# Kernel optimization log

Measured on AMD Instinct MI355X. Metric: run time of the kernel, lower is better.

## Reference

```python
import jax, jax.numpy as jnp
import numpy as np

N = 50000
R = 8
E = 100000
D_IN = 768
D_H = 256
LN_EPS = 1e-5


def _layer_norm(h, g, b):
    mu = jnp.mean(h, axis=-1, keepdims=True)
    var = jnp.mean((h - mu) ** 2, axis=-1, keepdims=True)
    return (h - mu) * jax.lax.rsqrt(var + LN_EPS) * g + b


def _rgcn_layer(x, node_w, edge_src, edge_tgt, W_rel, W_self_w, W_self_b, ln_g, ln_b):
    # x: [N, d_in]; edge_src/edge_tgt: [R, E]; W_rel: [R, d_in, d_out]
    n = x.shape[0]
    out = x @ W_self_w + W_self_b  # self loop
    for r in range(W_rel.shape[0]):  # fixed, small relation count
        src = edge_src[r]
        tgt = edge_tgt[r]
        feats = x[src] * node_w[src][:, None]          # gather + nuclearity scale, [E, d_in]
        msg = feats @ W_rel[r]                          # per-relation linear, [E, d_out]
        agg = jax.ops.segment_sum(msg, tgt, num_segments=n)                 # scatter_add
        cnt = jax.ops.segment_sum(jnp.ones(src.shape[0], x.dtype), tgt, num_segments=n)
        out = out + agg / jnp.clip(cnt, 1.0)[:, None]  # mean over relation neighbors
    return _layer_norm(jax.nn.relu(out), ln_g, ln_b)   # dropout = identity (eval)


def setup_inputs() -> dict:
    key = jax.random.key(0)
    ks = jax.random.split(key, 10)
    x = jax.random.normal(ks[0], (N, D_IN), dtype=jnp.float32)
    node_weights = jax.random.uniform(ks[1], (N,), dtype=jnp.float32)
    edge_src = jax.random.randint(ks[2], (R, E), 0, N, dtype=jnp.int32)
    edge_tgt = jax.random.randint(ks[3], (R, E), 0, N, dtype=jnp.int32)
    W_rel0 = jax.random.normal(ks[4], (R, D_IN, D_H), dtype=jnp.float32) / np.sqrt(D_IN)
    W_self0_w = jax.random.normal(ks[5], (D_IN, D_H), dtype=jnp.float32) / np.sqrt(D_IN)
    W_self0_b = jnp.zeros((D_H,), jnp.float32)
    W_rel1 = jax.random.normal(ks[6], (R, D_H, D_H), dtype=jnp.float32) / np.sqrt(D_H)
    W_self1_w = jax.random.normal(ks[7], (D_H, D_H), dtype=jnp.float32) / np.sqrt(D_H)
    W_self1_b = jnp.zeros((D_H,), jnp.float32)
    ones = jnp.ones((D_H,), jnp.float32)
    zeros = jnp.zeros((D_H,), jnp.float32)
    return {
        "x": x, "node_weights": node_weights,
        "edge_src": edge_src, "edge_tgt": edge_tgt,
        "W_rel0": W_rel0, "W_self0_w": W_self0_w, "W_self0_b": W_self0_b,
        "ln0_g": ones, "ln0_b": zeros,
        "W_rel1": W_rel1, "W_self1_w": W_self1_w, "W_self1_b": W_self1_b,
        "ln1_g": ones, "ln1_b": zeros,
    }


def reference(x, node_weights, edge_src, edge_tgt,
              W_rel0, W_self0_w, W_self0_b, ln0_g, ln0_b,
              W_rel1, W_self1_w, W_self1_b, ln1_g, ln1_b):
    h = _rgcn_layer(x, node_weights, edge_src, edge_tgt,
                    W_rel0, W_self0_w, W_self0_b, ln0_g, ln0_b)
    h = _rgcn_layer(h, node_weights, edge_src, edge_tgt,
                    W_rel1, W_self1_w, W_self1_b, ln1_g, ln1_b)
    return h  # [N, 256]
```

## Files before the change

kernel.cpp:

```cpp
#include <hip/hip_runtime.h>
#include <stdint.h>

#define N_NODES 50000
#define M_PAD   50048
#define R_REL   8
#define E_EDGES 100000
#define D_IN    768
#define D_H     256
#define N_CAT   2304
#define LN_EPS  1e-5f

#define TILES_N 18
#define TILES_M 391
#define T_TOT   (TILES_N * TILES_M)
#define T_PER_XCD ((T_TOT + 7) / 8)
#define NCHUNK  49

typedef __attribute__((ext_vector_type(8))) __bf16        bf16x8;
typedef __attribute__((ext_vector_type(4))) float         f32x4;
typedef __attribute__((ext_vector_type(8))) unsigned short u16x8;
typedef __attribute__((ext_vector_type(4))) unsigned short u16x4;
typedef __attribute__((ext_vector_type(4))) int            i32x4;

__device__ __forceinline__ float bf2f(unsigned short u) {
  union { float f; uint32_t i; } c; c.i = ((uint32_t)u) << 16; return c.f;
}
__device__ __forceinline__ unsigned short f2bf(float f) {
  uint32_t x = __float_as_uint(f);
  uint32_t r = (x + 0x7fffu + ((x >> 16) & 1u)) >> 16;
  return (unsigned short)r;
}

__device__ __forceinline__ void gload_lds16(const void* g, uint32_t lds_off) {
  __builtin_amdgcn_global_load_lds(
      (const __attribute__((address_space(1))) void*)(uintptr_t)g,
      (__attribute__((address_space(3))) void*)(uintptr_t)lds_off, 16, 0, 0);
}

__global__ void k_deg(const int* __restrict__ tgt, int* __restrict__ deg) {
  int e = blockIdx.x * 256 + threadIdx.x;
  if (e >= R_REL * E_EDGES) return;
  int r = e / E_EDGES;
  atomicAdd(&deg[r * N_NODES + tgt[e]], 1);
}

__global__ __launch_bounds__(256)
void k_scan1(const int* __restrict__ deg, int* __restrict__ rowptr,
             int* __restrict__ bsum) {
  __shared__ int wtot[4];
  const int r = blockIdx.y, chunk = blockIdx.x, tid = threadIdx.x;
  const int wave = tid >> 6, lane = tid & 63;
  const int i0 = chunk * 1024 + tid * 4;
  int v0 = 0, v1 = 0, v2 = 0, v3 = 0;
  const int* d = deg + r * N_NODES;
  if (chunk != NCHUNK - 1) {
    i32x4 v = *(const i32x4*)(d + i0);
    v0 = v[0]; v1 = v[1]; v2 = v[2]; v3 = v[3];
  } else {
    if (i0 + 0 < N_NODES) v0 = d[i0 + 0];
    if (i0 + 1 < N_NODES) v1 = d[i0 + 1];
    if (i0 + 2 < N_NODES) v2 = d[i0 + 2];
    if (i0 + 3 < N_NODES) v3 = d[i0 + 3];
  }
  const int tsum = v0 + v1 + v2 + v3;
  int inc = tsum;
#pragma unroll
  for (int off = 1; off < 64; off <<= 1) {
    int t = __shfl_up(inc, off, 64);
    if (lane >= off) inc += t;
  }
  if (lane == 63) wtot[wave] = inc;
  __syncthreads();
  int woff = 0;
#pragma unroll
  for (int w = 0; w < 4; ++w) woff += (w < wave) ? wtot[w] : 0;
  int excl = woff + inc - tsum;
  int* rp = rowptr + r * (N_NODES + 1);
  if (i0 + 0 < N_NODES) rp[i0 + 0] = excl;
  if (i0 + 1 < N_NODES) rp[i0 + 1] = excl + v0;
  if (i0 + 2 < N_NODES) rp[i0 + 2] = excl + v0 + v1;
  if (i0 + 3 < N_NODES) rp[i0 + 3] = excl + v0 + v1 + v2;
  if (tid == 0) bsum[r * NCHUNK + chunk] = wtot[0] + wtot[1] + wtot[2] + wtot[3];
}

__global__ __launch_bounds__(512)
void k_scan2(const int* __restrict__ bsum, int* __restrict__ chunkoff,
             int* __restrict__ rowptr) {
  const int r = threadIdx.x >> 6, lane = threadIdx.x & 63;
  int v = (lane < NCHUNK) ? bsum[r * NCHUNK + lane] : 0;
  int inc = v;
#pragma unroll
  for (int off = 1; off < 64; off <<= 1) {
    int t = __shfl_up(inc, off, 64);
    if (lane >= off) inc += t;
  }
  if (lane < NCHUNK) chunkoff[r * NCHUNK + lane] = inc - v;
  if (lane == NCHUNK - 1) rowptr[r * (N_NODES + 1) + N_NODES] = inc;
}

__global__ __launch_bounds__(256)
void k_scan3(const int* __restrict__ chunkoff, int* __restrict__ rowptr) {
  const int r = blockIdx.y, chunk = blockIdx.x;
  if (chunk == 0) return;
  const int off = chunkoff[r * NCHUNK + chunk];
  const int i0 = chunk * 1024 + threadIdx.x * 4;
  int* rp = rowptr + r * (N_NODES + 1);
#pragma unroll
  for (int j = 0; j < 4; ++j)
    if (i0 + j < N_NODES) rp[i0 + j] += off;
}

__global__ void k_fill(const int* __restrict__ src, const int* __restrict__ tgt,
                       const float* __restrict__ nw, const int* __restrict__ rowptr,
                       int* __restrict__ cursor, int2* __restrict__ e2) {
  int e = blockIdx.x * 256 + threadIdx.x;
  if (e >= R_REL * E_EDGES) return;
  int r = e / E_EDGES;
  int t = tgt[e], s = src[e];
  int pos = atomicAdd(&cursor[r * N_NODES + t], 1);
  int slot = r * E_EDGES + rowptr[r * (N_NODES + 1) + t] + pos;
  e2[slot] = make_int2(s, __float_as_int(nw[s]));
}

__global__ void k_cvt_x(const float* __restrict__ x, unsigned short* __restrict__ xb) {
  const size_t i = ((size_t)blockIdx.x * 256 + threadIdx.x) * 4;
  if (i >= (size_t)N_NODES * D_IN) return;
  const f32x4 v = *(const f32x4*)(x + i);
  u16x4 o = { f2bf(v[0]), f2bf(v[1]), f2bf(v[2]), f2bf(v[3]) };
  *(u16x4*)(xb + i) = o;
}

__global__ void k_cvt_w(const float* __restrict__ Ws, const float* __restrict__ Wr,
                        unsigned short* __restrict__ Wt, int K) {
  int idx = blockIdx.x * 256 + threadIdx.x;
  if (idx >= N_CAT * K) return;
  int n = idx / K, k = idx - n * K;
  float v = (n < 256) ? Ws[k * 256 + n]
                      : Wr[(size_t)((n - 256) >> 8) * K * 256 + k * 256 + (n & 255)];
  Wt[idx] = f2bf(v);
}

__global__ __launch_bounds__(256, 2)
void k_gemm(const unsigned short* __restrict__ A, const unsigned short* __restrict__ Bt,
            unsigned short* __restrict__ C, int K) {
  const int tile = (blockIdx.x & 7) * T_PER_XCD + (blockIdx.x >> 3);
  if (tile >= T_TOT) return;
  const int tileM = (tile / TILES_N) * 128;
  const int tileN = (tile % TILES_N) * 128;

  __shared__ __align__(16) char smem[32768];
  const int tid  = threadIdx.x;
  const int wave = tid >> 6, lane = tid & 63;
  const int wm = (wave >> 1) * 64, wn = (wave & 1) * 64;

  f32x4 acc[4][4] = {};

  const int srow = wave * 32 + (lane >> 2);
  const int kchunk = ((lane & 3) - ((lane >> 2) & 3)) & 3;
  const unsigned short* gA = A  + (size_t)(tileM + srow) * K + kchunk * 8;
  const unsigned short* gB = Bt + (size_t)(tileN + srow) * K + kchunk * 8;
  const uint32_t ldsA = (uint32_t)(uintptr_t)smem;
  const uint32_t ldsB = ldsA + 8192;
  const uint32_t lA0 = ldsA + (wave * 32) * 64;
  const uint32_t lB0 = ldsB + (wave * 32) * 64;
  const size_t rowstep = (size_t)16 * K;

  const int slot = (((lane >> 4) + (lane & 3)) & 3) * 16;
  const char* pA = smem        + (wm + (lane & 15)) * 64 + slot;
  const char* pB = smem + 8192 + (wn + (lane & 15)) * 64 + slot;

  const int nk = K >> 5;
  for (int kt = 0; kt < nk; ++kt) {
    const int koff = kt * 32;
    __syncthreads();
    gload_lds16(gA + koff,           lA0);
    gload_lds16(gA + rowstep + koff, lA0 + 16 * 64);
    gload_lds16(gB + koff,           lB0);
    gload_lds16(gB + rowstep + koff, lB0 + 16 * 64);
    __syncthreads();
    bf16x8 af[4], bfr[4];
#pragma unroll
    for (int i = 0; i < 4; ++i) af[i]  = *(const bf16x8*)(pA + i * 1024);
#pragma unroll
    for (int j = 0; j < 4; ++j) bfr[j] = *(const bf16x8*)(pB + j * 1024);
#pragma unroll
    for (int i = 0; i < 4; ++i)
#pragma unroll
      for (int j = 0; j < 4; ++j)
        acc[i][j] = __builtin_amdgcn_mfma_f32_16x16x32_bf16(af[i], bfr[j], acc[i][j], 0, 0, 0);
  }

  __syncthreads();
  unsigned short* st = (unsigned short*)smem + wave * 4096;
  const int rq = (lane >> 4) * 4, cq = lane & 15;
#pragma unroll
  for (int i = 0; i < 4; ++i)
#pragma unroll
    for (int j = 0; j < 4; ++j)
#pragma unroll
      for (int p = 0; p < 4; ++p)
        st[(i * 16 + rq + p) * 64 + j * 16 + cq] = f2bf(acc[i][j][p]);
  __syncthreads();
#pragma unroll
  for (int pass = 0; pass < 8; ++pass) {
    const int row = pass * 8 + (lane >> 3);
    u16x8 v = *(const u16x8*)(st + row * 64 + (lane & 7) * 8);
    size_t off = (size_t)(tileM + wm + row) * N_CAT + tileN + wn + (lane & 7) * 8;
    *(u16x8*)(C + off) = v;
  }
}

template <int FINAL>
__global__ __launch_bounds__(256)
void k_gather_ln(const unsigned short* __restrict__ Y, const int* __restrict__ rowptr,
                 const int2* __restrict__ e2, const float* __restrict__ bias,
                 const float* __restrict__ g, const float* __restrict__ bln,
                 void* __restrict__ out) {
  const int wave = threadIdx.x >> 6, lane = threadIdx.x & 63;
  const int t = blockIdx.x * 4 + wave;
  if (t >= N_NODES) return;
  const int c0 = lane * 4;

  float a0, a1, a2, a3;
  {
    u16x4 sv = *(const u16x4*)(Y + (size_t)t * N_CAT + c0);
    a0 = bf2f(sv[0]) + bias[c0 + 0];
    a1 = bf2f(sv[1]) + bias[c0 + 1];
    a2 = bf2f(sv[2]) + bias[c0 + 2];
    a3 = bf2f(sv[3]) + bias[c0 + 3];
  }
#pragma unroll
  for (int r = 0; r < R_REL; ++r) {
    const int rp0 = rowptr[r * (N_NODES + 1) + t];
    const int rp1 = rowptr[r * (N_NODES + 1) + t + 1];
    if (rp0 == rp1) continue;
    float r0 = 0, r1 = 0, r2 = 0, r3 = 0;
    float q0 = 0, q1 = 0, q2 = 0, q3 = 0;
    const int base = r * E_EDGES;
    const size_t colr = (size_t)(1 + r) * 256 + c0;
    int idx = rp0;
    for (; idx + 2 <= rp1; idx += 2) {
      const int2 p0 = e2[base + idx];
      const int2 p1 = e2[base + idx + 1];
      const float w0 = __int_as_float(p0.y);
      const float w1 = __int_as_float(p1.y);
      u16x4 v0 = *(const u16x4*)(Y + (size_t)p0.x * N_CAT + colr);
      u16x4 v1 = *(const u16x4*)(Y + (size_t)p1.x * N_CAT + colr);
      r0 += w0 * bf2f(v0[0]); r1 += w0 * bf2f(v0[1]);
      r2 += w0 * bf2f(v0[2]); r3 += w0 * bf2f(v0[3]);
      q0 += w1 * bf2f(v1[0]); q1 += w1 * bf2f(v1[1]);
      q2 += w1 * bf2f(v1[2]); q3 += w1 * bf2f(v1[3]);
    }
    if (idx < rp1) {
      const int2 p0 = e2[base + idx];
      const float w0 = __int_as_float(p0.y);
      u16x4 v0 = *(const u16x4*)(Y + (size_t)p0.x * N_CAT + colr);
      r0 += w0 * bf2f(v0[0]); r1 += w0 * bf2f(v0[1]);
      r2 += w0 * bf2f(v0[2]); r3 += w0 * bf2f(v0[3]);
    }
    const float inv = 1.0f / (float)(rp1 - rp0);
    a0 += inv * (r0 + q0); a1 += inv * (r1 + q1);
    a2 += inv * (r2 + q2); a3 += inv * (r3 + q3);
  }
  a0 = fmaxf(a0, 0.f); a1 = fmaxf(a1, 0.f); a2 = fmaxf(a2, 0.f); a3 = fmaxf(a3, 0.f);

  float s1 = a0 + a1 + a2 + a3;
#pragma unroll
  for (int off = 32; off > 0; off >>= 1) s1 += __shfl_xor(s1, off, 64);
  const float mu = s1 * (1.f / 256.f);
  const float d0 = a0 - mu, d1 = a1 - mu, d2 = a2 - mu, d3 = a3 - mu;
  float s2 = d0 * d0 + d1 * d1 + d2 * d2 + d3 * d3;
#pragma unroll
  for (int off = 32; off > 0; off >>= 1) s2 += __shfl_xor(s2, off, 64);
  const float rs = rsqrtf(s2 * (1.f / 256.f) + LN_EPS);
  const float o0 = d0 * rs * g[c0 + 0] + bln[c0 + 0];
  const float o1 = d1 * rs * g[c0 + 1] + bln[c0 + 1];
  const float o2 = d2 * rs * g[c0 + 2] + bln[c0 + 2];
  const float o3 = d3 * rs * g[c0 + 3] + bln[c0 + 3];
  if (FINAL) {
    f32x4 o = { o0, o1, o2, o3 };
    *(f32x4*)((float*)out + (size_t)t * 256 + c0) = o;
  } else {
    u16x4 o = { f2bf(o0), f2bf(o1), f2bf(o2), f2bf(o3) };
    *(u16x4*)((unsigned short*)out + (size_t)t * 256 + c0) = o;
  }
}

extern "C" void kernel_launch(void* const* d_in, const int* in_sizes, int n_in,
                              void* d_out, int out_size, void* d_ws, size_t ws_size,
                              hipStream_t stream) {
  (void)in_sizes; (void)n_in; (void)out_size; (void)ws_size;
  const float* x   = (const float*)d_in[0];
  const float* nw  = (const float*)d_in[1];
  const int*   esrc = (const int*)d_in[2];
  const int*   etgt = (const int*)d_in[3];
  const float* Wr0 = (const float*)d_in[4];
  const float* Ws0 = (const float*)d_in[5];
  const float* Wb0 = (const float*)d_in[6];
  const float* g0  = (const float*)d_in[7];
  const float* b0  = (const float*)d_in[8];
  const float* Wr1 = (const float*)d_in[9];
  const float* Ws1 = (const float*)d_in[10];
  const float* Wb1 = (const float*)d_in[11];
  const float* g1  = (const float*)d_in[12];
  const float* b1  = (const float*)d_in[13];

  char* p = (char*)d_ws;
  auto carve = [&](size_t bytes) {
    char* q = p;
    p += (bytes + 511) & ~(size_t)511;
    return q;
  };
  unsigned short* Y   = (unsigned short*)carve((size_t)M_PAD * N_CAT * 2);
  unsigned short* xb  = (unsigned short*)carve((size_t)M_PAD * D_IN * 2);
  unsigned short* h   = (unsigned short*)carve((size_t)M_PAD * D_H * 2);
  unsigned short* Wt0 = (unsigned short*)carve((size_t)N_CAT * D_IN * 2);
  unsigned short* Wt1 = (unsigned short*)carve((size_t)N_CAT * D_H * 2);
  int*   deg     = (int*)carve((size_t)R_REL * N_NODES * 4);
  int*   cursor  = (int*)carve((size_t)R_REL * N_NODES * 4);
  int*   rowptr  = (int*)carve((size_t)R_REL * (N_NODES + 1) * 4);
  int*   bsum    = (int*)carve((size_t)R_REL * NCHUNK * 4);
  int*   chunkoff= (int*)carve((size_t)R_REL * NCHUNK * 4);
  int2*  e2      = (int2*)carve((size_t)R_REL * E_EDGES * 8);

  hipMemsetAsync(deg, 0, (size_t)R_REL * N_NODES * 4, stream);
  hipMemsetAsync(cursor, 0, (size_t)R_REL * N_NODES * 4, stream);
  k_deg<<<(R_REL * E_EDGES + 255) / 256, 256, 0, stream>>>(etgt, deg);
  k_scan1<<<dim3(NCHUNK, R_REL), 256, 0, stream>>>(deg, rowptr, bsum);
  k_scan2<<<1, 512, 0, stream>>>(bsum, chunkoff, rowptr);
  k_scan3<<<dim3(NCHUNK, R_REL), 256, 0, stream>>>(chunkoff, rowptr);
  k_fill<<<(R_REL * E_EDGES + 255) / 256, 256, 0, stream>>>(esrc, etgt, nw, rowptr,
                                                            cursor, e2);
  k_cvt_x<<<(N_NODES * D_IN / 4 + 255) / 256, 256, 0, stream>>>(x, xb);
  k_cvt_w<<<(N_CAT * D_IN + 255) / 256, 256, 0, stream>>>(Ws0, Wr0, Wt0, D_IN);
  k_cvt_w<<<(N_CAT * D_H + 255) / 256, 256, 0, stream>>>(Ws1, Wr1, Wt1, D_H);

  const int nblk = 8 * T_PER_XCD;
  k_gemm<<<nblk, 256, 0, stream>>>(xb, Wt0, Y, D_IN);
  k_gather_ln<0><<<N_NODES / 4, 256, 0, stream>>>(Y, rowptr, e2, Wb0, g0, b0, h);
  k_gemm<<<nblk, 256, 0, stream>>>(h, Wt1, Y, D_H);
  k_gather_ln<1><<<N_NODES / 4, 256, 0, stream>>>(Y, rowptr, e2, Wb1, g1, b1, d_out);
}
```

Measured before the change: 894.7 us.

## Split gather wave into edge halves, pack row offsets, pad GEMM epilogue LDS

The gather/LayerNorm kernel now splits each wave into two halves. Each half processes alternate edges with 16-byte loads covering 8 columns per lane, and the halves are combined with one cross-half shuffle. A new prep kernel packs per-node (rowptr, degree) pairs for all relations contiguously, so each node reads its offsets from one cache line instead of strided rowptr arrays. The GEMM epilogue pads the LDS staging stride to 68 to avoid bank conflicts and drops a block-wide barrier, since each wave only reads back its own region. This adds one small kernel and a little LDS, and the half-wave split leaves half the lanes idle on edge-poor relations.

Measured after the change: 918.7 us. 1.03x slower.

```diff
diff --git a/kernel.cpp b/kernel.cpp
--- a/kernel.cpp
+++ b/kernel.cpp
@@ -15,6 +15,7 @@
 #define T_TOT   (TILES_N * TILES_M)
 #define T_PER_XCD ((T_TOT + 7) / 8)
 #define NCHUNK  49
+#define EP_STRIDE 68
 
 typedef __attribute__((ext_vector_type(8))) __bf16        bf16x8;
 typedef __attribute__((ext_vector_type(4))) float         f32x4;
@@ -110,6 +111,14 @@
     if (i0 + j < N_NODES) rp[i0 + j] += off;
 }
 
+__global__ void k_prep(const int* __restrict__ rowptr, const int* __restrict__ deg,
+                       int2* __restrict__ sc) {
+  int i = blockIdx.x * 256 + threadIdx.x;
+  if (i >= N_NODES * 8) return;
+  int t = i >> 3, r = i & 7;
+  sc[i] = make_int2(rowptr[r * (N_NODES + 1) + t], deg[r * N_NODES + t]);
+}
+
 __global__ void k_fill(const int* __restrict__ src, const int* __restrict__ tgt,
                        const float* __restrict__ nw, const int* __restrict__ rowptr,
                        int* __restrict__ cursor, int2* __restrict__ e2) {
@@ -148,7 +157,7 @@
   const int tileM = (tile / TILES_N) * 128;
   const int tileN = (tile % TILES_N) * 128;
 
-  __shared__ __align__(16) char smem[32768];
+  __shared__ __align__(16) char smem[34816];
   const int tid  = threadIdx.x;
   const int wave = tid >> 6, lane = tid & 63;
   const int wm = (wave >> 1) * 64, wn = (wave & 1) * 64;
@@ -191,7 +200,7 @@
   }
 
   __syncthreads();
-  unsigned short* st = (unsigned short*)smem + wave * 4096;
+  unsigned short* st = (unsigned short*)smem + wave * (64 * EP_STRIDE);
   const int rq = (lane >> 4) * 4, cq = lane & 15;
 #pragma unroll
   for (int i = 0; i < 4; ++i)
@@ -199,12 +208,14 @@
     for (int j = 0; j < 4; ++j)
 #pragma unroll
       for (int p = 0; p < 4; ++p)
-        st[(i * 16 + rq + p) * 64 + j * 16 + cq] = f2bf(acc[i][j][p]);
-  __syncthreads();
+        st[(i * 16 + rq + p) * EP_STRIDE + j * 16 + cq] = f2bf(acc[i][j][p]);
 #pragma unroll
   for (int pass = 0; pass < 8; ++pass) {
     const int row = pass * 8 + (lane >> 3);
-    u16x8 v = *(const u16x8*)(st + row * 64 + (lane & 7) * 8);
+    const unsigned short* rp_ = st + row * EP_STRIDE + (lane & 7) * 8;
+    u16x4 lo = *(const u16x4*)(rp_);
+    u16x4 hi = *(const u16x4*)(rp_ + 4);
+    u16x8 v = { lo[0], lo[1], lo[2], lo[3], hi[0], hi[1], hi[2], hi[3] };
     size_t off = (size_t)(tileM + wm + row) * N_CAT + tileN + wn + (lane & 7) * 8;
     *(u16x8*)(C + off) = v;
   }
@@ -212,77 +223,85 @@
 
 template <int FINAL>
 __global__ __launch_bounds__(256)
-void k_gather_ln(const unsigned short* __restrict__ Y, const int* __restrict__ rowptr,
+void k_gather_ln(const unsigned short* __restrict__ Y, const int2* __restrict__ sc,
                  const int2* __restrict__ e2, const float* __restrict__ bias,
                  const float* __restrict__ g, const float* __restrict__ bln,
                  void* __restrict__ out) {
   const int wave = threadIdx.x >> 6, lane = threadIdx.x & 63;
   const int t = blockIdx.x * 4 + wave;
   if (t >= N_NODES) return;
-  const int c0 = lane * 4;
-
-  float a0, a1, a2, a3;
-  {
-    u16x4 sv = *(const u16x4*)(Y + (size_t)t * N_CAT + c0);
-    a0 = bf2f(sv[0]) + bias[c0 + 0];
-    a1 = bf2f(sv[1]) + bias[c0 + 1];
-    a2 = bf2f(sv[2]) + bias[c0 + 2];
-    a3 = bf2f(sv[3]) + bias[c0 + 3];
-  }
+  const int h = lane >> 5, sl = lane & 31;
+  const int c0 = sl * 8;
+
+  float a[8];
+  if (h == 0) {
+    u16x8 sv = *(const u16x8*)(Y + (size_t)t * N_CAT + c0);
+#pragma unroll
+    for (int i = 0; i < 8; ++i) a[i] = bf2f(sv[i]);
+  } else {
+    f32x4 b0 = *(const f32x4*)(bias + c0);
+    f32x4 b1 = *(const f32x4*)(bias + c0 + 4);
+    a[0] = b0[0]; a[1] = b0[1]; a[2] = b0[2]; a[3] = b0[3];
+    a[4] = b1[0]; a[5] = b1[1]; a[6] = b1[2]; a[7] = b1[3];
+  }
+
 #pragma unroll
   for (int r = 0; r < R_REL; ++r) {
-    const int rp0 = rowptr[r * (N_NODES + 1) + t];
-    const int rp1 = rowptr[r * (N_NODES + 1) + t + 1];
-    if (rp0 == rp1) continue;
-    float r0 = 0, r1 = 0, r2 = 0, r3 = 0;
-    float q0 = 0, q1 = 0, q2 = 0, q3 = 0;
-    const int base = r * E_EDGES;
+    const int2 s = sc[t * 8 + r];
+    if (s.y == 0) continue;
+    const int base = r * E_EDGES + s.x;
     const size_t colr = (size_t)(1 + r) * 256 + c0;
-    int idx = rp0;
-    for (; idx + 2 <= rp1; idx += 2) {
-      const int2 p0 = e2[base + idx];
-      const int2 p1 = e2[base + idx + 1];
-      const float w0 = __int_as_float(p0.y);
-      const float w1 = __int_as_float(p1.y);
-      u16x4 v0 = *(const u16x4*)(Y + (size_t)p0.x * N_CAT + colr);
-      u16x4 v1 = *(const u16x4*)(Y + (size_t)p1.x * N_CAT + colr);
-      r0 += w0 * bf2f(v0[0]); r1 += w0 * bf2f(v0[1]);
-      r2 += w0 * bf2f(v0[2]); r3 += w0 * bf2f(v0[3]);
-      q0 += w1 * bf2f(v1[0]); q1 += w1 * bf2f(v1[1]);
-      q2 += w1 * bf2f(v1[2]); q3 += w1 * bf2f(v1[3]);
+    float acc[8] = {0, 0, 0, 0, 0, 0, 0, 0};
+    for (int idx = h; idx < s.y; idx += 2) {
+      const int2 p = e2[base + idx];
+      const float w = __int_as_float(p.y);
+      u16x8 v = *(const u16x8*)(Y + (size_t)p.x * N_CAT + colr);
+#pragma unroll
+      for (int i = 0; i < 8; ++i) acc[i] += w * bf2f(v[i]);
     }
-    if (idx < rp1) {
-      const int2 p0 = e2[base + idx];
-      const float w0 = __int_as_float(p0.y);
-      u16x4 v0 = *(const u16x4*)(Y + (size_t)p0.x * N_CAT + colr);
-      r0 += w0 * bf2f(v0[0]); r1 += w0 * bf2f(v0[1]);
-      r2 += w0 * bf2f(v0[2]); r3 += w0 * bf2f(v0[3]);
+    const float inv = 1.0f / (float)s.y;
+#pragma unroll
+    for (int i = 0; i < 8; ++i) a[i] += inv * acc[i];
+  }
+
+#pragma unroll
+  for (int i = 0; i < 8; ++i) {
+    a[i] += __shfl_xor(a[i], 32, 64);
+    a[i] = fmaxf(a[i], 0.f);
+  }
+  float s1 = ((a[0] + a[1]) + (a[2] + a[3])) + ((a[4] + a[5]) + (a[6] + a[7]));
+#pragma unroll
+  for (int off = 16; off > 0; off >>= 1) s1 += __shfl_xor(s1, off, 64);
+  const float mu = s1 * (1.f / 256.f);
+  float d[8], s2 = 0.f;
+#pragma unroll
+  for (int i = 0; i < 8; ++i) { d[i] = a[i] - mu; s2 += d[i] * d[i]; }
+#pragma unroll
+  for (int off = 16; off > 0; off >>= 1) s2 += __shfl_xor(s2, off, 64);
+  const float rs = rsqrtf(s2 * (1.f / 256.f) + LN_EPS);
+
+  f32x4 g0 = *(const f32x4*)(g + c0);
+  f32x4 g1 = *(const f32x4*)(g + c0 + 4);
+  f32x4 l0 = *(const f32x4*)(bln + c0);
+  f32x4 l1 = *(const f32x4*)(bln + c0 + 4);
+  float o[8];
+  o[0] = d[0] * rs * g0[0] + l0[0]; o[1] = d[1] * rs * g0[1] + l0[1];
+  o[2] = d[2] * rs * g0[2] + l0[2]; o[3] = d[3] * rs * g0[3] + l0[3];
+  o[4] = d[4] * rs * g1[0] + l1[0]; o[5] = d[5] * rs * g1[1] + l1[1];
+  o[6] = d[6] * rs * g1[2] + l1[2]; o[7] = d[7] * rs * g1[3] + l1[3];
+
+  if (h == 0) {
+    if (FINAL) {
+      float* op = (float*)out + (size_t)t * 256 + c0;
+      f32x4 v0 = { o[0], o[1], o[2], o[3] };
+      f32x4 v1 = { o[4], o[5], o[6], o[7] };
+      *(f32x4*)(op) = v0;
+      *(f32x4*)(op + 4) = v1;
+    } else {
+      u16x8 v = { f2bf(o[0]), f2bf(o[1]), f2bf(o[2]), f2bf(o[3]),
+                  f2bf(o[4]), f2bf(o[5]), f2bf(o[6]), f2bf(o[7]) };
+      *(u16x8*)((unsigned short*)out + (size_t)t * 256 + c0) = v;
     }
-    const float inv = 1.0f / (float)(rp1 - rp0);
-    a0 += inv * (r0 + q0); a1 += inv * (r1 + q1);
-    a2 += inv * (r2 + q2); a3 += inv * (r3 + q3);
-  }
-  a0 = fmaxf(a0, 0.f); a1 = fmaxf(a1, 0.f); a2 = fmaxf(a2, 0.f); a3 = fmaxf(a3, 0.f);
-
-  float s1 = a0 + a1 + a2 + a3;
-#pragma unroll
-  for (int off = 32; off > 0; off >>= 1) s1 += __shfl_xor(s1, off, 64);
-  const float mu = s1 * (1.f / 256.f);
-  const float d0 = a0 - mu, d1 = a1 - mu, d2 = a2 - mu, d3 = a3 - mu;
-  float s2 = d0 * d0 + d1 * d1 + d2 * d2 + d3 * d3;
-#pragma unroll
-  for (int off = 32; off > 0; off >>= 1) s2 += __shfl_xor(s2, off, 64);
-  const float rs = rsqrtf(s2 * (1.f / 256.f) + LN_EPS);
-  const float o0 = d0 * rs * g[c0 + 0] + bln[c0 + 0];
-  const float o1 = d1 * rs * g[c0 + 1] + bln[c0 + 1];
-  const float o2 = d2 * rs * g[c0 + 2] + bln[c0 + 2];
-  const float o3 = d3 * rs * g[c0 + 3] + bln[c0 + 3];
-  if (FINAL) {
-    f32x4 o = { o0, o1, o2, o3 };
-    *(f32x4*)((float*)out + (size_t)t * 256 + c0) = o;
-  } else {
-    u16x4 o = { f2bf(o0), f2bf(o1), f2bf(o2), f2bf(o3) };
-    *(u16x4*)((unsigned short*)out + (size_t)t * 256 + c0) = o;
   }
 }
 
@@ -322,6 +341,7 @@
   int*   bsum    = (int*)carve((size_t)R_REL * NCHUNK * 4);
   int*   chunkoff= (int*)carve((size_t)R_REL * NCHUNK * 4);
   int2*  e2      = (int2*)carve((size_t)R_REL * E_EDGES * 8);
+  int2*  sc      = (int2*)carve((size_t)N_NODES * 8 * 8);
 
   hipMemsetAsync(deg, 0, (size_t)R_REL * N_NODES * 4, stream);
   hipMemsetAsync(cursor, 0, (size_t)R_REL * N_NODES * 4, stream);
@@ -329,6 +349,7 @@
   k_scan1<<<dim3(NCHUNK, R_REL), 256, 0, stream>>>(deg, rowptr, bsum);
   k_scan2<<<1, 512, 0, stream>>>(bsum, chunkoff, rowptr);
   k_scan3<<<dim3(NCHUNK, R_REL), 256, 0, stream>>>(chunkoff, rowptr);
+  k_prep<<<(N_NODES * 8 + 255) / 256, 256, 0, stream>>>(rowptr, deg, sc);
   k_fill<<<(R_REL * E_EDGES + 255) / 256, 256, 0, stream>>>(esrc, etgt, nw, rowptr,
                                                             cursor, e2);
   k_cvt_x<<<(N_NODES * D_IN / 4 + 255) / 256, 256, 0, stream>>>(x, xb);
@@ -337,7 +358,7 @@
 
   const int nblk = 8 * T_PER_XCD;
   k_gemm<<<nblk, 256, 0, stream>>>(xb, Wt0, Y, D_IN);
-  k_gather_ln<0><<<N_NODES / 4, 256, 0, stream>>>(Y, rowptr, e2, Wb0, g0, b0, h);
+  k_gather_ln<0><<<N_NODES / 4, 256, 0, stream>>>(Y, sc, e2, Wb0, g0, b0, h);
   k_gemm<<<nblk, 256, 0, stream>>>(h, Wt1, Y, D_H);
-  k_gather_ln<1><<<N_NODES / 4, 256, 0, stream>>>(Y, rowptr, e2, Wb1, g1, b1, d_out);
-}
+  k_gather_ln<1><<<N_NODES / 4, 256, 0, stream>>>(Y, sc, e2, Wb1, g1, b1, d_out);
+}
```
